# Kernel tuning notes

Measured on AMD Instinct MI355X. Metric: run time of the kernel, lower is better.

Reference implementation:

```python
import jax, jax.numpy as jnp
import numpy as np

N_NODES = 50000
N_EDGES = 1_600_000
N_REL = 8
D_IN = 128
D_OUT = 128


def _unique_edges(rng, n_nodes, n_rel, n_edges):
    # Torch module clamps the dense adjacency to 0/1, so duplicate
    # (rel, src, dst) triples collapse; generate unique edges so the
    # edge-list formulation matches exactly.
    m = 2 * n_edges
    src = rng.integers(0, n_nodes, m)
    dst = rng.integers(0, n_nodes, m)
    et = rng.integers(0, n_rel, m)
    key = (et.astype(np.int64) * n_nodes + src) * n_nodes + dst
    _, idx = np.unique(key, return_index=True)
    idx = np.sort(idx)[:n_edges]
    return src[idx], dst[idx], et[idx]


def setup_inputs() -> dict:
    key = jax.random.key(0)
    kx, kw, kr, kb = jax.random.split(key, 4)
    rng = np.random.default_rng(0)
    src, dst, et = _unique_edges(rng, N_NODES, N_REL, N_EDGES)
    bound = 1.0 / np.sqrt(D_OUT)
    return {
        "x": jax.random.normal(kx, (N_NODES, D_IN), dtype=jnp.float32),
        "edge_index": jnp.asarray(np.stack([src, dst]), dtype=jnp.int64),
        "edge_type": jnp.asarray(et, dtype=jnp.int64),
        "weight": jax.random.uniform(kw, (N_REL, D_OUT, D_IN), minval=-bound, maxval=bound, dtype=jnp.float32),
        "root": jax.random.uniform(kr, (D_OUT, D_IN), minval=-bound, maxval=bound, dtype=jnp.float32),
        "bias": jax.random.uniform(kb, (D_OUT,), minval=-bound, maxval=bound, dtype=jnp.float32),
    }


def reference(x, edge_index, edge_type, weight, root, bias):
    # Math identical to: adj[l, src, dst] = 1; adj row-normalized (mean);
    # out = sum_r norm_adj_r @ x @ W_r^T + x @ root^T + bias.
    n_rel, d_out, d_in = weight.shape
    n_nodes = x.shape[0]
    src = edge_index[0]
    dst = edge_index[1]
    seg = (edge_type * n_nodes + src).astype(jnp.int32)  # segment per (rel, node)
    num_seg = n_rel * n_nodes
    # sum of neighbor features per (relation, node): [R*N, d_in]
    agg = jax.ops.segment_sum(x[dst], seg, num_segments=num_seg)
    deg = jax.ops.segment_sum(jnp.ones((src.shape[0],), dtype=x.dtype), seg, num_segments=num_seg)
    norm = jnp.where(deg > 0, 1.0 / deg, 0.0)[:, None]  # mean aggr, nan_to_num(0)
    agg = (agg * norm).reshape(n_rel, n_nodes, d_in)
    out = jnp.einsum('rnd,rod->no', agg, weight)
    out = out + x @ root.T + bias[None]
    return out
```

## Files before the change

### kernel.cpp

```cpp
#include <hip/hip_runtime.h>


#define D 128
#define SCAN_CHUNK 2048
#define SEG_BITS 9
#define SEGS_PER_BUCKET 512
#define NBLK 128
#define NDEG 32

typedef __attribute__((ext_vector_type(8))) short short8;
typedef __attribute__((ext_vector_type(4))) float v4f;
typedef __attribute__((ext_vector_type(2))) float f32x2;
typedef __attribute__((ext_vector_type(4))) unsigned uint4v;

#define GLOAD_LDS16(gptr, lptr) \
    __builtin_amdgcn_global_load_lds((const __attribute__((address_space(1))) void*)(gptr), \
                                     (__attribute__((address_space(3))) void*)(lptr), 16, 0, 0)

__device__ __forceinline__ unsigned short f2b(float f) {
    union { float f; unsigned u; } v; v.f = f;
    unsigned r = v.u + 0x7fffu + ((v.u >> 16) & 1u);
    return (unsigned short)(r >> 16);
}
__device__ __forceinline__ float blo(unsigned u) {
    union { unsigned u; float f; } v; v.u = u << 16; return v.f;
}
__device__ __forceinline__ float bhi(unsigned u) {
    union { unsigned u; float f; } v; v.u = u & 0xffff0000u; return v.f;
}

__global__ void cvt_bf16_all(const float* __restrict__ x, long long nx,
                             const float* __restrict__ w, long long nw,
                             const float* __restrict__ root, long long nr,
                             unsigned short* __restrict__ xB,
                             unsigned short* __restrict__ xRow,
                             unsigned short* __restrict__ wB, int nN) {
    long long i = ((long long)blockIdx.x * blockDim.x + threadIdx.x) * 4;
    if (i < nx) {
        float4 v = *(const float4*)(x + i);
        uint2 p;
        p.x = (unsigned)f2b(v.x) | ((unsigned)f2b(v.y) << 16);
        p.y = (unsigned)f2b(v.z) | ((unsigned)f2b(v.w) << 16);
        long long n = i >> 7;
        int d = (int)(i & 127);
        size_t o = (size_t)(d >> 5) * (size_t)nN * 32 + (size_t)n * 32 + (d & 31);
        *(uint2*)(xB + o) = p;
        *(uint2*)(xRow + i) = p;
        return;
    }
    const float* src;
    unsigned short* dst;
    long long j;
    if (i < nx + nw) { src = w; dst = wB; j = i - nx; }
    else if (i < nx + nw + nr) { src = root; dst = wB + nw; j = i - nx - nw; }
    else return;
    float4 v = *(const float4*)(src + j);
    uint2 p;
    p.x = (unsigned)f2b(v.x) | ((unsigned)f2b(v.y) << 16);
    p.y = (unsigned)f2b(v.z) | ((unsigned)f2b(v.w) << 16);
    *(uint2*)(dst + j) = p;
}

__global__ __launch_bounds__(256)
void histA(const int* __restrict__ ei, const int* __restrict__ et,
           int* __restrict__ blockHist, int nE, int nN, int B, int epb) {
    __shared__ int lh[1024];
    const int tid = threadIdx.x;
    for (int b = tid; b < B; b += 256) lh[b] = 0;
    __syncthreads();
    const int base = blockIdx.x * epb;
    const int lim = min(base + epb, nE);
    for (int e = base + tid; e < lim; e += 256) {
        int seg = et[e] * nN + ei[e];
        atomicAdd(&lh[seg >> SEG_BITS], 1);
    }
    __syncthreads();
    for (int b = tid; b < B; b += 256)
        blockHist[b * NBLK + blockIdx.x] = lh[b];
}

__global__ __launch_bounds__(256)
void scan1(const int* __restrict__ in, int* __restrict__ excl,
           int* __restrict__ blockSums, int n) {
    __shared__ int t[256];
    const int tid = threadIdx.x;
    const int base = blockIdx.x * SCAN_CHUNK + tid * 8;
    int v[8];
    int tot = 0;
#pragma unroll
    for (int i = 0; i < 8; i++) {
        v[i] = (base + i < n) ? in[base + i] : 0;
        tot += v[i];
    }
    t[tid] = tot;
    __syncthreads();
    for (int off = 1; off < 256; off <<= 1) {
        int add = (tid >= off) ? t[tid - off] : 0;
        __syncthreads();
        t[tid] += add;
        __syncthreads();
    }
    int run = t[tid] - tot;
#pragma unroll
    for (int i = 0; i < 8; i++) {
        if (base + i < n) excl[base + i] = run;
        run += v[i];
    }
    if (tid == 255) blockSums[blockIdx.x] = t[255];
}

__global__ __launch_bounds__(256)
void scan2(int* __restrict__ blockSums, int nb) {
    __shared__ int t[256];
    const int tid = threadIdx.x;
    int v = (tid < nb) ? blockSums[tid] : 0;
    t[tid] = v;
    __syncthreads();
    for (int off = 1; off < 256; off <<= 1) {
        int add = (tid >= off) ? t[tid - off] : 0;
        __syncthreads();
        t[tid] += add;
        __syncthreads();
    }
    if (tid < nb) blockSums[tid] = t[tid] - v;
}

__global__ __launch_bounds__(256)
void scatterA(const int* __restrict__ ei, const int* __restrict__ et,
              const int* __restrict__ scanned, const int* __restrict__ blockSums,
              unsigned* __restrict__ bucketEdges,
              int nE, int nN, int B, int epb) {
    __shared__ int cur[1024];
    const int tid = threadIdx.x;
    for (int b = tid; b < B; b += 256) {
        int idx = b * NBLK + blockIdx.x;
        cur[b] = scanned[idx] + blockSums[idx >> 11];
    }
    __syncthreads();
    const int base = blockIdx.x * epb;
    const int lim = min(base + epb, nE);
    for (int e = base + tid; e < lim; e += 256) {
        int seg = et[e] * nN + ei[e];
        int bkt = seg >> SEG_BITS;
        unsigned pk = ((unsigned)(seg & (SEGS_PER_BUCKET - 1)) << 16) | (unsigned)ei[nE + e];
        int pos = atomicAdd(&cur[bkt], 1);
        bucketEdges[pos] = pk;
    }
}

__global__ __launch_bounds__(256)
void segOff(const unsigned* __restrict__ bucketEdges, const int* __restrict__ scanned,
            const int* __restrict__ blockSums,
            int4* __restrict__ permRec, unsigned short* __restrict__ sortedDst,
            int* __restrict__ permMax, int nE, int numSeg, int B) {
    __shared__ int lh[SEGS_PER_BUCKET];
    __shared__ int sc[256];
    __shared__ int lcur[SEGS_PER_BUCKET];
    __shared__ int dcnt[256];
    __shared__ int dbase[256];
    __shared__ int smax[32];
    const int tid = threadIdx.x;
    const int b = blockIdx.x;
    const int i0 = b * NBLK;
    const int eBase = scanned[i0] + blockSums[i0 >> 11];
    int eEnd = nE;
    if (b + 1 < B) {
        const int i1 = (b + 1) * NBLK;
        eEnd = scanned[i1] + blockSums[i1 >> 11];
    }
    const int segBase = b * SEGS_PER_BUCKET;
    const int segLim = min(SEGS_PER_BUCKET, numSeg - segBase);

    lh[2 * tid] = 0; lh[2 * tid + 1] = 0;
    dcnt[tid] = 0;
    if (tid < 32) smax[tid] = 0;
    __syncthreads();
    for (int i = eBase + tid; i < eEnd; i += 256)
        atomicAdd(&lh[bucketEdges[i] >> 16], 1);
    __syncthreads();
    const int li0 = 2 * tid, li1 = 2 * tid + 1;
    const int sub = li0 >> 6;
    int a0 = lh[li0], a1 = lh[li1];
    int b0 = min(a0, NDEG - 1), b1 = min(a1, NDEG - 1), r0 = 0, r1 = 0;
    if (li0 < segLim) r0 = atomicAdd(&dcnt[sub * NDEG + b0], 1);
    if (li1 < segLim) r1 = atomicAdd(&dcnt[sub * NDEG + b1], 1);
    sc[tid] = a0 + a1;
    __syncthreads();
    for (int o = 1; o < 256; o <<= 1) {
        int add = (tid >= o) ? sc[tid - o] : 0;
        __syncthreads();
        sc[tid] += add;
        __syncthreads();
    }
    int pairBase = sc[tid] - (a0 + a1);
    int g0 = eBase + pairBase;
    int g1 = g0 + a0;
    lcur[li0] = g0;
    lcur[li1] = g1;
    if (tid < 8) {
        int run = 0;
#pragma unroll
        for (int k = 0; k < NDEG; k++) { dbase[tid * NDEG + k] = run; run += dcnt[tid * NDEG + k]; }
    }
    __syncthreads();
    if (li0 < segLim) {
        int rk = dbase[sub * NDEG + b0] + r0;
        permRec[segBase + sub * 64 + rk] = make_int4(g0, a0, segBase + li0, 0);
        atomicMax(&smax[(sub << 2) + (rk >> 4)], a0);
    }
    if (li1 < segLim) {
        int rk = dbase[sub * NDEG + b1] + r1;
        permRec[segBase + sub * 64 + rk] = make_int4(g1, a1, segBase + li1, 0);
        atomicMax(&smax[(sub << 2) + (rk >> 4)], a1);
    }
    for (int i = eBase + tid; i < eEnd; i += 256) {
        unsigned u = bucketEdges[i];
        int pos = atomicAdd(&lcur[u >> 16], 1);
        sortedDst[pos] = (unsigned short)(u & 0xFFFFu);
    }
    __syncthreads();
    if (tid < 32) permMax[b * 32 + tid] = smax[tid];
}

__global__ __launch_bounds__(256)
void rgcn_gather(const unsigned short* __restrict__ xB,
                 const unsigned short* __restrict__ sortedDst,
                 const int4* __restrict__ permRec,
                 const int* __restrict__ permMax,
                 unsigned short* __restrict__ Abuf, int nN, int numSeg,
                 size_t SL, unsigned long long M) {
    const int tid = threadIdx.x;
    const int lane = tid & 63;
    const int idx4 = lane & 3;
    const int grp = lane >> 2;
    const int wv = tid >> 6;
    const int gsi0 = blockIdx.x * 128 + wv * 32 + grp;
    const int gsi1 = gsi0 + 16;
    const int sl = blockIdx.y;
    const bool v0 = (gsi0 < numSeg);
    const bool v1 = (gsi1 < numSeg);

    int4 rc0 = v0 ? permRec[gsi0] : make_int4(0, 0, 0, 0);
    int4 rc1 = v1 ? permRec[gsi1] : make_int4(0, 0, 0, 0);
    int mx0 = v0 ? permMax[gsi0 >> 4] : 0;
    int mx1 = v1 ? permMax[gsi1 >> 4] : 0;
    mx0 = __builtin_amdgcn_readfirstlane(mx0);
    mx1 = __builtin_amdgcn_readfirstlane(mx1);

    const int start0 = rc0.x, cnt0 = v0 ? rc0.y : 0, seg0 = rc0.z;
    const int start1 = rc1.x, cnt1 = v1 ? rc1.y : 0, seg1 = rc1.z;

    f32x2 a0[4], a1[4];
#pragma unroll
    for (int i = 0; i < 4; i++) { a0[i] = (f32x2){0.f, 0.f}; a1[i] = (f32x2){0.f, 0.f}; }

    const unsigned short* xSlab = xB + (size_t)sl * nN * 32 + idx4 * 8;

    const int mxm = max(mx0, mx1);
    for (int b = 0; b < mxm; b += 4) {
        uint4v w0[4], w1[4];
        int myD0 = 0, myD1 = 0;
        if (b < mx0) myD0 = (b + idx4 < cnt0) ? (int)sortedDst[start0 + b + idx4] : 0;
        if (b < mx1) myD1 = (b + idx4 < cnt1) ? (int)sortedDst[start1 + b + idx4] : 0;
        if (b < mx0) {
#pragma unroll
            for (int j = 0; j < 4; j++) {
                int dst = __shfl(myD0, grp * 4 + j);
                bool act = (b + j < cnt0);
                w0[j] = act ? *(const uint4v*)(xSlab + ((size_t)dst << 5))
                            : (uint4v){0u, 0u, 0u, 0u};
            }
        }
        if (b < mx1) {
#pragma unroll
            for (int j = 0; j < 4; j++) {
                int dst = __shfl(myD1, grp * 4 + j);
                bool act = (b + j < cnt1);
                w1[j] = act ? *(const uint4v*)(xSlab + ((size_t)dst << 5))
                            : (uint4v){0u, 0u, 0u, 0u};
            }
        }
        if (b < mx0) {
#pragma unroll
            for (int j = 0; j < 4; j++) {
                f32x2 t0 = (f32x2){blo(w0[j].x), bhi(w0[j].x)};
                f32x2 t1 = (f32x2){blo(w0[j].y), bhi(w0[j].y)};
                f32x2 t2 = (f32x2){blo(w0[j].z), bhi(w0[j].z)};
                f32x2 t3 = (f32x2){blo(w0[j].w), bhi(w0[j].w)};
                asm("v_pk_add_f32 %0, %0, %1" : "+v"(a0[0]) : "v"(t0));
                asm("v_pk_add_f32 %0, %0, %1" : "+v"(a0[1]) : "v"(t1));
                asm("v_pk_add_f32 %0, %0, %1" : "+v"(a0[2]) : "v"(t2));
                asm("v_pk_add_f32 %0, %0, %1" : "+v"(a0[3]) : "v"(t3));
            }
        }
        if (b < mx1) {
#pragma unroll
            for (int j = 0; j < 4; j++) {
                f32x2 t0 = (f32x2){blo(w1[j].x), bhi(w1[j].x)};
                f32x2 t1 = (f32x2){blo(w1[j].y), bhi(w1[j].y)};
                f32x2 t2 = (f32x2){blo(w1[j].z), bhi(w1[j].z)};
                f32x2 t3 = (f32x2){blo(w1[j].w), bhi(w1[j].w)};
                asm("v_pk_add_f32 %0, %0, %1" : "+v"(a1[0]) : "v"(t0));
                asm("v_pk_add_f32 %0, %0, %1" : "+v"(a1[1]) : "v"(t1));
                asm("v_pk_add_f32 %0, %0, %1" : "+v"(a1[2]) : "v"(t2));
                asm("v_pk_add_f32 %0, %0, %1" : "+v"(a1[3]) : "v"(t3));
            }
        }
    }

    if (v0) {
        float s = cnt0 > 0 ? 1.0f / (float)cnt0 : 0.f;
        const int r = (int)(((unsigned long long)seg0 * M) >> 48);
        const int n = seg0 - r * nN;
        unsigned p0, p1, p2, p3;
        float e0, e1;
        e0 = a0[0].x * s; e1 = a0[0].y * s;
        asm("v_cvt_pk_bf16_f32 %0, %1, %2" : "=v"(p0) : "v"(e0), "v"(e1));
        e0 = a0[1].x * s; e1 = a0[1].y * s;
        asm("v_cvt_pk_bf16_f32 %0, %1, %2" : "=v"(p1) : "v"(e0), "v"(e1));
        e0 = a0[2].x * s; e1 = a0[2].y * s;
        asm("v_cvt_pk_bf16_f32 %0, %1, %2" : "=v"(p2) : "v"(e0), "v"(e1));
        e0 = a0[3].x * s; e1 = a0[3].y * s;
        asm("v_cvt_pk_bf16_f32 %0, %1, %2" : "=v"(p3) : "v"(e0), "v"(e1));
        uint4v pkt = (uint4v){p0, p1, p2, p3};
        __builtin_nontemporal_store(pkt,
            (uint4v*)(Abuf + (size_t)r * SL + (size_t)n * D + sl * 32 + idx4 * 8));
    }
    if (v1) {
        float s = cnt1 > 0 ? 1.0f / (float)cnt1 : 0.f;
        const int r = (int)(((unsigned long long)seg1 * M) >> 48);
        const int n = seg1 - r * nN;
        unsigned p0, p1, p2, p3;
        float e0, e1;
        e0 = a1[0].x * s; e1 = a1[0].y * s;
        asm("v_cvt_pk_bf16_f32 %0, %1, %2" : "=v"(p0) : "v"(e0), "v"(e1));
        e0 = a1[1].x * s; e1 = a1[1].y * s;
        asm("v_cvt_pk_bf16_f32 %0, %1, %2" : "=v"(p1) : "v"(e0), "v"(e1));
        e0 = a1[2].x * s; e1 = a1[2].y * s;
        asm("v_cvt_pk_bf16_f32 %0, %1, %2" : "=v"(p2) : "v"(e0), "v"(e1));
        e0 = a1[3].x * s; e1 = a1[3].y * s;
        asm("v_cvt_pk_bf16_f32 %0, %1, %2" : "=v"(p3) : "v"(e0), "v"(e1));
        uint4v pkt = (uint4v){p0, p1, p2, p3};
        __builtin_nontemporal_store(pkt,
            (uint4v*)(Abuf + (size_t)r * SL + (size_t)n * D + sl * 32 + idx4 * 8));
    }
}

__global__ __launch_bounds__(256)
void rgcn_gemm_mfma(const unsigned short* __restrict__ A,
                    const unsigned short* __restrict__ wB,
                    const float* __restrict__ bias,
                    float* __restrict__ out, int nN, int nRel, size_t SL) {
    __shared__ __align__(16) unsigned short As[2][64 * 64];
    __shared__ __align__(16) unsigned short Bs[2][128 * 64];
    const int tid = threadIdx.x;
    const int wave = tid >> 6;
    const int lane = tid & 63;
    const int wm = wave & 1;
    const int wn = wave >> 1;
    const int m16 = lane & 15;
    const int q = lane >> 4;
    const int row0 = blockIdx.x * 64;

    v4f acc[2][4];
#pragma unroll
    for (int i = 0; i < 2; i++)
#pragma unroll
        for (int j = 0; j < 4; j++) acc[i][j] = (v4f){0.f, 0.f, 0.f, 0.f};

    const int sw = m16 & 7;
    int aoff[2][2], boff[4][2];
#pragma unroll
    for (int mt = 0; mt < 2; mt++) {
        int row = wm * 32 + mt * 16 + m16;
#pragma unroll
        for (int kb = 0; kb < 2; kb++)
            aoff[mt][kb] = row * 64 + (((kb * 4 + q) ^ sw) * 8);
    }
#pragma unroll
    for (int nt = 0; nt < 4; nt++) {
        int o = wn * 64 + nt * 16 + m16;
#pragma unroll
        for (int kb = 0; kb < 2; kb++)
            boff[nt][kb] = o * 64 + (((kb * 4 + q) ^ sw) * 8);
    }

    const int l8 = lane >> 3;
    const int gd = (lane & 7) ^ l8;
    const size_t aBase = (size_t)(row0 + wave * 16 + l8) * D + gd * 8;
    const size_t bBase = (size_t)(wave * 32 + l8) * D + gd * 8;

    const int nT = 2 * (nRel + 1);

#define STAGE(buf, t) do { \
        const int s_ = (t) >> 1, h_ = (t) & 1; \
        const unsigned short* ga_ = A + (size_t)s_ * SL + h_ * 64 + aBase; \
        const unsigned short* gb_ = wB + (size_t)s_ * (D * D) + h_ * 64 + bBase; \
        GLOAD_LDS16(ga_,        &As[buf][(wave * 2 + 0) * 512]); \
        GLOAD_LDS16(ga_ + 1024, &As[buf][(wave * 2 + 1) * 512]); \
        GLOAD_LDS16(gb_,        &Bs[buf][(wave * 4 + 0) * 512]); \
        GLOAD_LDS16(gb_ + 1024, &Bs[buf][(wave * 4 + 1) * 512]); \
        GLOAD_LDS16(gb_ + 2048, &Bs[buf][(wave * 4 + 2) * 512]); \
        GLOAD_LDS16(gb_ + 3072, &Bs[buf][(wave * 4 + 3) * 512]); \
    } while (0)

    STAGE(0, 0);
    __syncthreads();
    int cur = 0;
    for (int t = 0; t < nT; ++t) {
        if (t + 1 < nT) STAGE(cur ^ 1, t + 1);
        const unsigned short* Ab = As[cur];
        const unsigned short* Bb = Bs[cur];
        short8 a[2][2], b[4][2];
#pragma unroll
        for (int kb = 0; kb < 2; kb++) {
#pragma unroll
            for (int mt = 0; mt < 2; mt++)
                a[mt][kb] = *(const short8*)&Ab[aoff[mt][kb]];
#pragma unroll
            for (int nt = 0; nt < 4; nt++)
                b[nt][kb] = *(const short8*)&Bb[boff[nt][kb]];
        }
#pragma unroll
        for (int kb = 0; kb < 2; kb++)
#pragma unroll
            for (int mt = 0; mt < 2; mt++)
#pragma unroll
                for (int nt = 0; nt < 4; nt++)
                    acc[mt][nt] = __builtin_amdgcn_mfma_f32_16x16x32_bf16(
                        a[mt][kb], b[nt][kb], acc[mt][nt], 0, 0, 0);
        __syncthreads();
        cur ^= 1;
    }
#undef STAGE

#pragma unroll
    for (int mt = 0; mt < 2; mt++) {
#pragma unroll
        for (int nt = 0; nt < 4; nt++) {
            int col = wn * 64 + nt * 16 + m16;
            float bi = bias[col];
#pragma unroll
            for (int reg = 0; reg < 4; reg++) {
                int rrow = row0 + wm * 32 + mt * 16 + q * 4 + reg;
                if (rrow < nN)
                    out[(size_t)rrow * D + col] = acc[mt][nt][reg] + bi;
            }
        }
    }
}

extern "C" void kernel_launch(void* const* d_in, const int* in_sizes, int n_in,
                              void* d_out, int out_size, void* d_ws, size_t ws_size,
                              hipStream_t stream) {
    const float* x    = (const float*)d_in[0];
    const int*   ei   = (const int*)d_in[1];
    const int*   et   = (const int*)d_in[2];
    const float* w    = (const float*)d_in[3];
    const float* root = (const float*)d_in[4];
    const float* bias = (const float*)d_in[5];
    float* out = (float*)d_out;

    const int nN   = in_sizes[0] / D;
    const int nE   = in_sizes[2];
    const int nRel = in_sizes[3] / (D * D);
    const int numSeg = nRel * nN;
    const int B = (numSeg + SEGS_PER_BUCKET - 1) >> SEG_BITS;
    const int nBH = B * NBLK;
    const int epb = (nE + NBLK - 1) / NBLK;
    const int nNalloc = (nN + 63) & ~63;
    const size_t SL = (size_t)nNalloc * D;
    const unsigned long long M = ((1ULL << 48) + nN - 1) / nN;

    char* p = (char*)d_ws;
    unsigned* bucketEdges   = (unsigned*)p;        p += (size_t)nE * sizeof(unsigned);
    unsigned short* sortedDst = (unsigned short*)p; p += (size_t)nE * sizeof(unsigned short);
    p = (char*)(((uintptr_t)p + 255) & ~(uintptr_t)255);
    int* blockHist = (int*)p;  p += (size_t)nBH * sizeof(int);
    int* scanned   = (int*)p;  p += (size_t)nBH * sizeof(int);
    int* blockSums = (int*)p;  p += 256 * sizeof(int);
    p = (char*)(((uintptr_t)p + 255) & ~(uintptr_t)255);
    int4* permRec  = (int4*)p; p += (size_t)numSeg * sizeof(int4);
    int* permMax   = (int*)p;  p += (size_t)B * 32 * sizeof(int);
    p = (char*)(((uintptr_t)p + 255) & ~(uintptr_t)255);
    unsigned short* xB   = (unsigned short*)p;  p += (size_t)nN * D * sizeof(unsigned short);
    unsigned short* wBc  = (unsigned short*)p;  p += (size_t)(nRel + 1) * D * D * sizeof(unsigned short);
    p = (char*)(((uintptr_t)p + 255) & ~(uintptr_t)255);
    unsigned short* Abuf = (unsigned short*)p;
    unsigned short* xRow = Abuf + (size_t)nRel * SL;

    const int nScanBlocks = (nBH + SCAN_CHUNK - 1) / SCAN_CHUNK;

    histA<<<NBLK, 256, 0, stream>>>(ei, et, blockHist, nE, nN, B, epb);
    scan1<<<nScanBlocks, 256, 0, stream>>>(blockHist, scanned, blockSums, nBH);
    scan2<<<1, 256, 0, stream>>>(blockSums, nScanBlocks);
    scatterA<<<NBLK, 256, 0, stream>>>(ei, et, scanned, blockSums, bucketEdges, nE, nN, B, epb);
    segOff<<<B, 256, 0, stream>>>(bucketEdges, scanned, blockSums, permRec, sortedDst, permMax,
                                  nE, numSeg, B);

    long long nx = (long long)nN * D;
    long long nw = (long long)nRel * D * D;
    long long nr = (long long)D * D;
    long long ncvt = (nx + nw + nr) / 4;
    cvt_bf16_all<<<(int)((ncvt + 255) / 256), 256, 0, stream>>>(x, nx, w, nw, root, nr,
                                                                xB, xRow, wBc, nN);

    dim3 gg((numSeg + 127) / 128, 4);
    rgcn_gather<<<gg, 256, 0, stream>>>(xB, sortedDst, permRec, permMax, Abuf, nN, numSeg, SL, M);

    rgcn_gemm_mfma<<<(nN + 63) / 64, 256, 0, stream>>>(Abuf, wBc, bias, out, nN, nRel, SL);
}
```

Before: 268.0 us.

## Store aggregated features in slab-major layout shared with bf16 x copy

Changes the Abuf layout to 32-column slabs indexed by (slab, relation), so the gather writes contiguous 64-byte rows per slab. The bf16 x copy is written directly as the ninth relation in each slab, removing the separate xB buffer and the duplicate xRow store. The GEMM's A-tile addressing is rewritten to match the new slab layout. This saves one full write of x and may improve gather write locality, but GEMM A loads now come from two slabs per half-tile instead of one contiguous row.

Measured after the change: 272.6 us. About the same (+1.7%).

```diff
diff --git a/kernel.cpp b/kernel.cpp
--- a/kernel.cpp
+++ b/kernel.cpp
@@ -32,9 +32,8 @@
 __global__ void cvt_bf16_all(const float* __restrict__ x, long long nx,
                              const float* __restrict__ w, long long nw,
                              const float* __restrict__ root, long long nr,
-                             unsigned short* __restrict__ xB,
-                             unsigned short* __restrict__ xRow,
-                             unsigned short* __restrict__ wB, int nN) {
+                             unsigned short* __restrict__ Abuf,
+                             unsigned short* __restrict__ wB, size_t SLs) {
     long long i = ((long long)blockIdx.x * blockDim.x + threadIdx.x) * 4;
     if (i < nx) {
         float4 v = *(const float4*)(x + i);
@@ -43,9 +42,8 @@
         p.y = (unsigned)f2b(v.z) | ((unsigned)f2b(v.w) << 16);
         long long n = i >> 7;
         int d = (int)(i & 127);
-        size_t o = (size_t)(d >> 5) * (size_t)nN * 32 + (size_t)n * 32 + (d & 31);
-        *(uint2*)(xB + o) = p;
-        *(uint2*)(xRow + i) = p;
+        size_t o = (size_t)((d >> 5) * 9 + 8) * SLs + (size_t)n * 32 + (d & 31);
+        *(uint2*)(Abuf + o) = p;
         return;
     }
     const float* src;
@@ -223,12 +221,12 @@
 }
 
 __global__ __launch_bounds__(256)
-void rgcn_gather(const unsigned short* __restrict__ xB,
+void rgcn_gather(const unsigned short* __restrict__ Abase,
                  const unsigned short* __restrict__ sortedDst,
                  const int4* __restrict__ permRec,
                  const int* __restrict__ permMax,
                  unsigned short* __restrict__ Abuf, int nN, int numSeg,
-                 size_t SL, unsigned long long M) {
+                 size_t SLs, unsigned long long M) {
     const int tid = threadIdx.x;
     const int lane = tid & 63;
     const int idx4 = lane & 3;
@@ -254,7 +252,7 @@
 #pragma unroll
     for (int i = 0; i < 4; i++) { a0[i] = (f32x2){0.f, 0.f}; a1[i] = (f32x2){0.f, 0.f}; }
 
-    const unsigned short* xSlab = xB + (size_t)sl * nN * 32 + idx4 * 8;
+    const unsigned short* xSlab = Abase + (size_t)(sl * 9 + 8) * SLs + idx4 * 8;
 
     const int mxm = max(mx0, mx1);
     for (int b = 0; b < mxm; b += 4) {
@@ -324,7 +322,7 @@
         asm("v_cvt_pk_bf16_f32 %0, %1, %2" : "=v"(p3) : "v"(e0), "v"(e1));
         uint4v pkt = (uint4v){p0, p1, p2, p3};
         __builtin_nontemporal_store(pkt,
-            (uint4v*)(Abuf + (size_t)r * SL + (size_t)n * D + sl * 32 + idx4 * 8));
+            (uint4v*)(Abuf + (size_t)(sl * 9 + r) * SLs + (size_t)n * 32 + idx4 * 8));
     }
     if (v1) {
         float s = cnt1 > 0 ? 1.0f / (float)cnt1 : 0.f;
@@ -342,7 +340,7 @@
         asm("v_cvt_pk_bf16_f32 %0, %1, %2" : "=v"(p3) : "v"(e0), "v"(e1));
         uint4v pkt = (uint4v){p0, p1, p2, p3};
         __builtin_nontemporal_store(pkt,
-            (uint4v*)(Abuf + (size_t)r * SL + (size_t)n * D + sl * 32 + idx4 * 8));
+            (uint4v*)(Abuf + (size_t)(sl * 9 + r) * SLs + (size_t)n * 32 + idx4 * 8));
     }
 }
 
@@ -350,7 +348,7 @@
 void rgcn_gemm_mfma(const unsigned short* __restrict__ A,
                     const unsigned short* __restrict__ wB,
                     const float* __restrict__ bias,
-                    float* __restrict__ out, int nN, int nRel, size_t SL) {
+                    float* __restrict__ out, int nN, int nRel, size_t SLs) {
     __shared__ __align__(16) unsigned short As[2][64 * 64];
     __shared__ __align__(16) unsigned short Bs[2][128 * 64];
     const int tid = threadIdx.x;
@@ -387,17 +385,18 @@
 
     const int l8 = lane >> 3;
     const int gd = (lane & 7) ^ l8;
-    const size_t aBase = (size_t)(row0 + wave * 16 + l8) * D + gd * 8;
+    const size_t aBaseH0 = (size_t)((gd >> 2) * 9) * SLs
+                         + (size_t)(row0 + wave * 16 + l8) * 32 + (gd & 3) * 8;
     const size_t bBase = (size_t)(wave * 32 + l8) * D + gd * 8;
 
     const int nT = 2 * (nRel + 1);
 
 #define STAGE(buf, t) do { \
         const int s_ = (t) >> 1, h_ = (t) & 1; \
-        const unsigned short* ga_ = A + (size_t)s_ * SL + h_ * 64 + aBase; \
+        const unsigned short* ga_ = A + aBaseH0 + (size_t)h_ * 18 * SLs + (size_t)s_ * SLs; \
         const unsigned short* gb_ = wB + (size_t)s_ * (D * D) + h_ * 64 + bBase; \
         GLOAD_LDS16(ga_,        &As[buf][(wave * 2 + 0) * 512]); \
-        GLOAD_LDS16(ga_ + 1024, &As[buf][(wave * 2 + 1) * 512]); \
+        GLOAD_LDS16(ga_ + 256,  &As[buf][(wave * 2 + 1) * 512]); \
         GLOAD_LDS16(gb_,        &Bs[buf][(wave * 4 + 0) * 512]); \
         GLOAD_LDS16(gb_ + 1024, &Bs[buf][(wave * 4 + 1) * 512]); \
         GLOAD_LDS16(gb_ + 2048, &Bs[buf][(wave * 4 + 2) * 512]); \
@@ -469,7 +468,7 @@
     const int nBH = B * NBLK;
     const int epb = (nE + NBLK - 1) / NBLK;
     const int nNalloc = (nN + 63) & ~63;
-    const size_t SL = (size_t)nNalloc * D;
+    const size_t SLs = (size_t)nNalloc * 32;
     const unsigned long long M = ((1ULL << 48) + nN - 1) / nN;
 
     char* p = (char*)d_ws;
@@ -483,11 +482,9 @@
     int4* permRec  = (int4*)p; p += (size_t)numSeg * sizeof(int4);
     int* permMax   = (int*)p;  p += (size_t)B * 32 * sizeof(int);
     p = (char*)(((uintptr_t)p + 255) & ~(uintptr_t)255);
-    unsigned short* xB   = (unsigned short*)p;  p += (size_t)nN * D * sizeof(unsigned short);
     unsigned short* wBc  = (unsigned short*)p;  p += (size_t)(nRel + 1) * D * D * sizeof(unsigned short);
     p = (char*)(((uintptr_t)p + 255) & ~(uintptr_t)255);
     unsigned short* Abuf = (unsigned short*)p;
-    unsigned short* xRow = Abuf + (size_t)nRel * SL;
 
     const int nScanBlocks = (nBH + SCAN_CHUNK - 1) / SCAN_CHUNK;
 
@@ -503,10 +500,11 @@
     long long nr = (long long)D * D;
     long long ncvt = (nx + nw + nr) / 4;
     cvt_bf16_all<<<(int)((ncvt + 255) / 256), 256, 0, stream>>>(x, nx, w, nw, root, nr,
-                                                                xB, xRow, wBc, nN);
+                                                                Abuf, wBc, SLs);
 
     dim3 gg((numSeg + 127) / 128, 4);
-    rgcn_gather<<<gg, 256, 0, stream>>>(xB, sortedDst, permRec, permMax, Abuf, nN, numSeg, SL, M);
-
-    rgcn_gemm_mfma<<<(nN + 63) / 64, 256, 0, stream>>>(Abuf, wBc, bias, out, nN, nRel, SL);
-}
+    rgcn_gather<<<gg, 256, 0, stream>>>(Abuf, sortedDst, permRec, permMax, Abuf, nN, numSeg,
+                                        SLs, M);
+
+    rgcn_gemm_mfma<<<(nN + 63) / 64, 256, 0, stream>>>(Abuf, wBc, bias, out, nN, nRel, SLs);
+}
```
